# Optimization experiments

Measured on AMD Instinct MI355X. Metric: run time of the kernel, lower is better.

The kernel has to match this reference:

```python
import jax, jax.numpy as jnp
import numpy as np
import math

B, T, D = 2, 2048, 1024
H, HS = 16, 64  # n_heads, head_size; D == H*HS


def setup_inputs() -> dict:
    key = jax.random.key(0)
    k1, k2, k3 = jax.random.split(key, 3)
    x = jax.random.normal(k1, (B, T, D), dtype=jnp.float32)
    w_qkv = jax.random.normal(k2, (D, 3 * D), dtype=jnp.float32) * (1.0 / math.sqrt(D))
    b_qkv = jnp.zeros((3 * D,), dtype=jnp.float32)
    w_out = jax.random.normal(k3, (D, D), dtype=jnp.float32) * (1.0 / math.sqrt(D))
    b_out = jnp.zeros((D,), dtype=jnp.float32)
    return {"x": x, "w_qkv": w_qkv, "b_qkv": b_qkv, "w_out": w_out, "b_out": b_out}


def reference(x, w_qkv, b_qkv, w_out, b_out):
    b, t, d = x.shape
    qkv = x @ w_qkv + b_qkv                       # (B,T,3D)
    q, k, v = jnp.split(qkv, 3, axis=-1)
    # (B,T,D) -> (B,H,T,HS)
    q = q.reshape(b, t, H, HS).transpose(0, 2, 1, 3)
    k = k.reshape(b, t, H, HS).transpose(0, 2, 1, 3)
    v = v.reshape(b, t, H, HS).transpose(0, 2, 1, 3)
    scale = 1.0 / math.sqrt(HS)
    attn = jnp.einsum('bhqd,bhkd->bhqk', q, k) * scale  # (B,H,T,T)
    causal = jnp.tril(jnp.ones((t, t), dtype=bool))
    attn = jnp.where(causal[None, None], attn, -jnp.inf)
    attn = jax.nn.softmax(attn, axis=-1)
    o = jnp.einsum('bhqk,bhkd->bhqd', attn, v)          # (B,H,T,HS)
    o = o.transpose(0, 2, 1, 3).reshape(b, t, d)
    return o @ w_out + b_out
```

## Files before the change

kernel.cpp:

```cpp
#include <hip/hip_runtime.h>
#include <math.h>

#define B_  2
#define T_  2048
#define D_  1024
#define H_  16
#define HS_ 64
#define M_  (B_*T_)

typedef __bf16 bf16x8 __attribute__((ext_vector_type(8)));
typedef float  f32x4  __attribute__((ext_vector_type(4)));
typedef unsigned short u16;

static __device__ __forceinline__ u16 f2bf(float f) {
    __bf16 h = (__bf16)f;
    return *reinterpret_cast<u16*>(&h);
}

static __device__ __forceinline__ void glds16(const u16* g, u16* l) {
    __builtin_amdgcn_global_load_lds(
        (const __attribute__((address_space(1))) void*)g,
        (__attribute__((address_space(3))) void*)l, 16, 0, 0);
}

__global__ __launch_bounds__(256) void prep_kernel(
    const float* __restrict__ x, const float* __restrict__ w_qkv,
    const float* __restrict__ w_out,
    u16* __restrict__ Xb, u16* __restrict__ WqkvT, u16* __restrict__ WoutT)
{
    int bid = blockIdx.x;
    if (bid < 4096) {
        int i = (bid * 256 + threadIdx.x) * 4;
        float4 v = *reinterpret_cast<const float4*>(x + i);
        ushort4 o;
        o.x = f2bf(v.x); o.y = f2bf(v.y); o.z = f2bf(v.z); o.w = f2bf(v.w);
        *reinterpret_cast<ushort4*>(Xb + i) = o;
        return;
    }
    const float* in; u16* out; int C; int c0, r0;
    if (bid < 4096 + 3072) {
        int t = bid - 4096;
        in = w_qkv; out = WqkvT; C = 3 * D_;
        c0 = (t % 96) * 32; r0 = (t / 96) * 32;
    } else {
        int t = bid - 7168;
        in = w_out; out = WoutT; C = D_;
        c0 = (t & 31) * 32; r0 = (t >> 5) * 32;
    }
    __shared__ float tile[32][33];
    int tr = threadIdx.x >> 3, tc4 = (threadIdx.x & 7) * 4;
    float4 v = *reinterpret_cast<const float4*>(in + (size_t)(r0 + tr) * C + c0 + tc4);
    tile[tr][tc4+0] = v.x; tile[tr][tc4+1] = v.y;
    tile[tr][tc4+2] = v.z; tile[tr][tc4+3] = v.w;
    __syncthreads();
    ushort4 o;
    o.x = f2bf(tile[tc4+0][tr]); o.y = f2bf(tile[tc4+1][tr]);
    o.z = f2bf(tile[tc4+2][tr]); o.w = f2bf(tile[tc4+3][tr]);
    *reinterpret_cast<ushort4*>(out + (size_t)(c0 + tr) * D_ + r0 + tc4) = o;
}

__global__ __launch_bounds__(512, 2) void gemm_qkv(
    const u16* __restrict__ A, const u16* __restrict__ Bt,
    const float* __restrict__ bias,
    u16* __restrict__ Qb, u16* __restrict__ Kb, u16* __restrict__ Vt)
{
    constexpr int K  = D_;
    constexpr int NT = K / 64;

    __shared__ u16 LDS[2][2][2][8192];

    const int tid  = threadIdx.x;
    const int lane = tid & 63, wave = tid >> 6;
    const int wm = wave >> 2, wn = wave & 3;
    const int quad = lane >> 4, lr = lane & 15;

    const int lin = blockIdx.x + 16 * blockIdx.y;
    const int xcd = lin & 7, rr = lin >> 3;
    const int bm = (xcd & 3) * 4 + (rr & 3);
    const int bn = (xcd >> 2) * 6 + (rr >> 2);

    const u16* Ab = A  + (size_t)(bm * 256) * K;
    const u16* Bb = Bt + (size_t)(bn * 256) * K;

    const int r0 = tid >> 2;
    const int c0 = (tid & 3) ^ ((tid >> 3) & 3);
    const u16* sA0 = Ab + (size_t)r0 * K + c0 * 8;
    const u16* sA1 = sA0 + (size_t)128 * K;
    const u16* sB0 = Bb + (size_t)r0 * K + c0 * 8;
    const u16* sB1 = sB0 + (size_t)128 * K;
    const int d0 = tid * 8, d1 = (tid + 512) * 8;

    const int swz = (lr >> 1) & 3;
    const int eA = ((wm*128 + lr) * 4 + (quad ^ swz)) * 8;
    const int eB = ((wn*64  + lr) * 4 + (quad ^ swz)) * 8;

    f32x4 acc[8][4] = {};

#define STG(mat, kh, tt) do { \
        u16* _d = &LDS[(tt) & 1][mat][kh][0]; \
        const int _ko = (tt) * 64 + (kh) * 32; \
        glds16(((mat) ? sB0 : sA0) + _ko, _d + d0); \
        glds16(((mat) ? sB1 : sA1) + _ko, _d + d1); \
    } while (0)

#define MFMA_QUAD(mh) do { \
        __builtin_amdgcn_s_setprio(1); \
        _Pragma("unroll") \
        for (int i_ = 0; i_ < 4; ++i_) \
            _Pragma("unroll") \
            for (int j_ = 0; j_ < 4; ++j_) \
                acc[(mh)*4 + i_][j_] = __builtin_amdgcn_mfma_f32_16x16x32_bf16( \
                    a[i_], b[j_], acc[(mh)*4 + i_][j_], 0, 0, 0); \
        __builtin_amdgcn_s_setprio(0); \
    } while (0)

    STG(0,0,0); STG(1,0,0); STG(0,1,0); STG(1,1,0);
    asm volatile("s_waitcnt vmcnt(4)" ::: "memory");
    __builtin_amdgcn_s_barrier();

    for (int t = 0; t < NT; ++t) {
        const int cb = t & 1;
        const bool last = (t == NT - 1);
        const u16* Ar0 = &LDS[cb][0][0][0];
        const u16* Ar1 = &LDS[cb][0][1][0];
        const u16* Br0 = &LDS[cb][1][0][0];
        const u16* Br1 = &LDS[cb][1][1][0];
        bf16x8 a[4], b[4];

        #pragma unroll
        for (int i = 0; i < 4; ++i) a[i] = *reinterpret_cast<const bf16x8*>(Ar0 + eA + i*512);
        #pragma unroll
        for (int j = 0; j < 4; ++j) b[j] = *reinterpret_cast<const bf16x8*>(Br0 + eB + j*512);
        if (!last) STG(0,0,t+1);
        __builtin_amdgcn_s_barrier();
        asm volatile("s_waitcnt lgkmcnt(0)" ::: "memory");
        MFMA_QUAD(0);
        __builtin_amdgcn_s_barrier();

        #pragma unroll
        for (int i = 0; i < 4; ++i) a[i] = *reinterpret_cast<const bf16x8*>(Ar0 + eA + (i+4)*512);
        if (!last) STG(1,0,t+1);
        __builtin_amdgcn_s_barrier();
        asm volatile("s_waitcnt lgkmcnt(0)" ::: "memory");
        MFMA_QUAD(1);
        if (!last) { asm volatile("s_waitcnt vmcnt(4)" ::: "memory"); }
        else       { asm volatile("s_waitcnt vmcnt(0)" ::: "memory"); }
        __builtin_amdgcn_s_barrier();

        #pragma unroll
        for (int i = 0; i < 4; ++i) a[i] = *reinterpret_cast<const bf16x8*>(Ar1 + eA + i*512);
        #pragma unroll
        for (int j = 0; j < 4; ++j) b[j] = *reinterpret_cast<const bf16x8*>(Br1 + eB + j*512);
        if (!last) STG(0,1,t+1);
        __builtin_amdgcn_s_barrier();
        asm volatile("s_waitcnt lgkmcnt(0)" ::: "memory");
        MFMA_QUAD(0);
        __builtin_amdgcn_s_barrier();

        #pragma unroll
        for (int i = 0; i < 4; ++i) a[i] = *reinterpret_cast<const bf16x8*>(Ar1 + eA + (i+4)*512);
        if (!last) STG(1,1,t+1);
        __builtin_amdgcn_s_barrier();
        asm volatile("s_waitcnt lgkmcnt(0)" ::: "memory");
        MFMA_QUAD(1);
        asm volatile("s_waitcnt vmcnt(4)" ::: "memory");
        __builtin_amdgcn_s_barrier();
    }
#undef STG
#undef MFMA_QUAD

    #pragma unroll
    for (int i = 0; i < 8; ++i) {
        int m0 = bm*256 + wm*128 + i*16 + quad*4;
        #pragma unroll
        for (int j = 0; j < 4; ++j) {
            int ncol = bn*256 + wn*64 + j*16 + lr;
            float bv = bias[ncol];
            float v4[4];
            #pragma unroll
            for (int r = 0; r < 4; ++r) v4[r] = acc[i][j][r] + bv;
            int bb = m0 >> 11, t0 = m0 & (T_ - 1);
            int s = ncol >> 10, rem = ncol & 1023;
            int h = rem >> 6, d = rem & 63;
            int bh = bb * H_ + h;
            if (s == 0) {
                #pragma unroll
                for (int r = 0; r < 4; ++r)
                    Qb[((size_t)bh*T_ + t0 + r)*HS_ + d] = f2bf(v4[r] * 0.1803368801111244f);
            } else if (s == 1) {
                #pragma unroll
                for (int r = 0; r < 4; ++r)
                    Kb[((size_t)bh*T_ + t0 + r)*HS_ + d] = f2bf(v4[r]);
            } else {
                ushort4 o;
                o.x = f2bf(v4[0]); o.y = f2bf(v4[1]);
                o.z = f2bf(v4[2]); o.w = f2bf(v4[3]);
                *reinterpret_cast<ushort4*>(&Vt[((size_t)bh*HS_ + d)*T_ + t0]) = o;
            }
        }
    }
}

__global__ __launch_bounds__(256, 2) void gemm_out(
    const u16* __restrict__ A, const u16* __restrict__ Bt,
    const float* __restrict__ bias, float* __restrict__ Cf)
{
    constexpr int K  = D_;
    constexpr int N  = D_;
    constexpr int NT = K / 64;

    __shared__ u16 LDS[2][2][2][4096];

    const int tid  = threadIdx.x;
    const int lane = tid & 63, wave = tid >> 6;
    const int wm = wave >> 1, wn = wave & 1;
    const int quad = lane >> 4, lr = lane & 15;
    const int bm = blockIdx.x, bn = blockIdx.y;

    const u16* Ab = A  + (size_t)(bm * 128) * K;
    const u16* Bb = Bt + (size_t)(bn * 128) * K;

    const int r0 = tid >> 2;
    const int c0 = (tid & 3) ^ ((tid >> 3) & 3);
    const u16* sA0 = Ab + (size_t)r0 * K + c0 * 8;
    const u16* sA1 = sA0 + (size_t)64 * K;
    const u16* sB0 = Bb + (size_t)r0 * K + c0 * 8;
    const u16* sB1 = sB0 + (size_t)64 * K;
    const int d0 = tid * 8, d1 = (tid + 256) * 8;

    const int swz = (lr >> 1) & 3;
    const int eA = ((wm*64 + lr) * 4 + (quad ^ swz)) * 8;
    const int eB = ((wn*64 + lr) * 4 + (quad ^ swz)) * 8;

    f32x4 acc[4][4] = {};

#define STGO(kh, tt) do { \
        const int _ko = (tt) * 64 + (kh) * 32; \
        glds16(sA0 + _ko, &LDS[(tt) & 1][0][kh][0] + d0); \
        glds16(sA1 + _ko, &LDS[(tt) & 1][0][kh][0] + d1); \
        glds16(sB0 + _ko, &LDS[(tt) & 1][1][kh][0] + d0); \
        glds16(sB1 + _ko, &LDS[(tt) & 1][1][kh][0] + d1); \
    } while (0)

    STGO(0, 0); STGO(1, 0);
    asm volatile("s_waitcnt vmcnt(4)" ::: "memory");
    __builtin_amdgcn_s_barrier();

    for (int t = 0; t < NT; ++t) {
        const int cb = t & 1;
        const bool last = (t == NT - 1);
        bf16x8 a[4], b[4];

        {
            const u16* Ar = &LDS[cb][0][0][0];
            const u16* Br = &LDS[cb][1][0][0];
            #pragma unroll
            for (int i = 0; i < 4; ++i) a[i] = *reinterpret_cast<const bf16x8*>(Ar + eA + i*512);
            #pragma unroll
            for (int j = 0; j < 4; ++j) b[j] = *reinterpret_cast<const bf16x8*>(Br + eB + j*512);
            if (!last) STGO(0, t+1);
            __builtin_amdgcn_s_barrier();
            asm volatile("s_waitcnt lgkmcnt(0)" ::: "memory");
            __builtin_amdgcn_s_setprio(1);
            #pragma unroll
            for (int i = 0; i < 4; ++i)
                #pragma unroll
                for (int j = 0; j < 4; ++j)
                    acc[i][j] = __builtin_amdgcn_mfma_f32_16x16x32_bf16(a[i], b[j], acc[i][j], 0, 0, 0);
            __builtin_amdgcn_s_setprio(0);
            if (!last) { asm volatile("s_waitcnt vmcnt(4)" ::: "memory"); }
            else       { asm volatile("s_waitcnt vmcnt(0)" ::: "memory"); }
            __builtin_amdgcn_s_barrier();
        }

        {
            const u16* Ar = &LDS[cb][0][1][0];
            const u16* Br = &LDS[cb][1][1][0];
            #pragma unroll
            for (int i = 0; i < 4; ++i) a[i] = *reinterpret_cast<const bf16x8*>(Ar + eA + i*512);
            #pragma unroll
            for (int j = 0; j < 4; ++j) b[j] = *reinterpret_cast<const bf16x8*>(Br + eB + j*512);
            if (!last) STGO(1, t+1);
            __builtin_amdgcn_s_barrier();
            asm volatile("s_waitcnt lgkmcnt(0)" ::: "memory");
            __builtin_amdgcn_s_setprio(1);
            #pragma unroll
            for (int i = 0; i < 4; ++i)
                #pragma unroll
                for (int j = 0; j < 4; ++j)
                    acc[i][j] = __builtin_amdgcn_mfma_f32_16x16x32_bf16(a[i], b[j], acc[i][j], 0, 0, 0);
            __builtin_amdgcn_s_setprio(0);
            if (!last) { asm volatile("s_waitcnt vmcnt(4)" ::: "memory"); }
            __builtin_amdgcn_s_barrier();
        }
    }
#undef STGO

    #pragma unroll
    for (int i = 0; i < 4; ++i) {
        int m0 = bm*128 + wm*64 + i*16 + quad*4;
        #pragma unroll
        for (int j = 0; j < 4; ++j) {
            int ncol = bn*128 + wn*64 + j*16 + lr;
            float bv = bias[ncol];
            #pragma unroll
            for (int r = 0; r < 4; ++r)
                Cf[(size_t)(m0 + r) * N + ncol] = acc[i][j][r] + bv;
        }
    }
}

__global__ __launch_bounds__(256) void attn_kernel(
    const u16* __restrict__ Qb, const u16* __restrict__ Kb,
    const u16* __restrict__ Vt, u16* __restrict__ Ob)
{
    __shared__ u16 Ks[64 * 64];
    __shared__ u16 Vs[64 * 64];
    __shared__ u16 Ps[4][2][16 * 64];

    int tid  = threadIdx.x;
    int lane = tid & 63, wave = tid >> 6;
    int quad = lane >> 4, lr = lane & 15;

    int lin = blockIdx.x;
    int bh  = (lin & 7) + 8 * ((lin >> 3) & 3);
    int p   = lin >> 5;
    int qlo = p, qhi = 31 - p;
    int rlo = qlo * 64 + wave * 16;
    int rhi = qhi * 64 + wave * 16;

    const u16* QpL = Qb + ((size_t)bh * T_ + rlo) * HS_;
    const u16* QpH = Qb + ((size_t)bh * T_ + rhi) * HS_;
    bf16x8 qfL[2], qfH[2];
    #pragma unroll
    for (int h2 = 0; h2 < 2; ++h2) {
        qfL[h2] = *reinterpret_cast<const bf16x8*>(QpL + lr*HS_ + h2*32 + quad*8);
        qfH[h2] = *reinterpret_cast<const bf16x8*>(QpH + lr*HS_ + h2*32 + quad*8);
    }

    f32x4 OaL[4] = {}, OaH[4] = {};
    float lrL[4] = {0.f,0.f,0.f,0.f}, lrH[4] = {0.f,0.f,0.f,0.f};

    int e   = quad ^ (lr & 7);
    int rb0 = (lr * 8 + e) * 8;
    int rb1 = (lr * 8 + (e ^ 4)) * 8;
    int offw[4][4];
    #pragma unroll
    for (int nt = 0; nt < 4; ++nt)
        #pragma unroll
        for (int r = 0; r < 4; ++r) {
            int prow = quad*4 + r;
            offw[nt][r] = (prow*8 + ((nt*2 + (lr >> 3)) ^ (prow & 7)))*8 + (lr & 7);
        }
    u16* PsL = Ps[wave][0];
    u16* PsH = Ps[wave][1];

    int srow = tid >> 3;
    int scol = ((tid & 7) ^ (srow & 7)) * 8;
    const u16* kp0 = Kb + ((size_t)bh*T_ + srow     )*HS_ + scol;
    const u16* kp1 = Kb + ((size_t)bh*T_ + srow + 32)*HS_ + scol;
    const u16* vp0 = Vt + ((size_t)bh*HS_ + srow     )*T_ + scol;
    const u16* vp1 = Vt + ((size_t)bh*HS_ + srow + 32)*T_ + scol;

    bf16x8 kpre0 = *reinterpret_cast<const bf16x8*>(kp0);
    bf16x8 kpre1 = *reinterpret_cast<const bf16x8*>(kp1);
    bf16x8 vpre0 = *reinterpret_cast<const bf16x8*>(vp0);
    bf16x8 vpre1 = *reinterpret_cast<const bf16x8*>(vp1);

    for (int jt = 0; jt <= qhi; ++jt) {
        __syncthreads();
        reinterpret_cast<bf16x8*>(Ks)[tid]       = kpre0;
        reinterpret_cast<bf16x8*>(Ks)[tid + 256] = kpre1;
        reinterpret_cast<bf16x8*>(Vs)[tid]       = vpre0;
        reinterpret_cast<bf16x8*>(Vs)[tid + 256] = vpre1;
        if (jt < qhi) {
            kp0 += 64*HS_; kp1 += 64*HS_; vp0 += 64; vp1 += 64;
            kpre0 = *reinterpret_cast<const bf16x8*>(kp0);
            kpre1 = *reinterpret_cast<const bf16x8*>(kp1);
            vpre0 = *reinterpret_cast<const bf16x8*>(vp0);
            vpre1 = *reinterpret_cast<const bf16x8*>(vp1);
        }
        __syncthreads();

        const bool lo = (jt <= qlo);

        f32x4 SaH[4] = {}, SaL[4] = {};
        __builtin_amdgcn_s_setprio(1);
        #pragma unroll
        for (int nt = 0; nt < 4; ++nt) {
            bf16x8 bk0 = *reinterpret_cast<const bf16x8*>(Ks + rb0 + nt*1024);
            bf16x8 bk1 = *reinterpret_cast<const bf16x8*>(Ks + rb1 + nt*1024);
            SaH[nt] = __builtin_amdgcn_mfma_f32_16x16x32_bf16(qfH[0], bk0, SaH[nt], 0, 0, 0);
            SaH[nt] = __builtin_amdgcn_mfma_f32_16x16x32_bf16(qfH[1], bk1, SaH[nt], 0, 0, 0);
        }
        if (lo) {
            #pragma unroll
            for (int nt = 0; nt < 4; ++nt) {
                bf16x8 bk0 = *reinterpret_cast<const bf16x8*>(Ks + rb0 + nt*1024);
                bf16x8 bk1 = *reinterpret_cast<const bf16x8*>(Ks + rb1 + nt*1024);
                SaL[nt] = __builtin_amdgcn_mfma_f32_16x16x32_bf16(qfL[0], bk0, SaL[nt], 0, 0, 0);
                SaL[nt] = __builtin_amdgcn_mfma_f32_16x16x32_bf16(qfL[1], bk1, SaL[nt], 0, 0, 0);
            }
        }
        __builtin_amdgcn_s_setprio(0);

        if (jt == qhi) {
            int kb = jt * 64;
            #pragma unroll
            for (int nt = 0; nt < 4; ++nt)
                #pragma unroll
                for (int r = 0; r < 4; ++r) {
                    int kg = kb + nt*16 + lr;
                    int qg = rhi + quad*4 + r;
                    if (kg > qg) SaH[nt][r] = -INFINITY;
                }
        }
        if (jt == qlo) {
            int kb = jt * 64;
            #pragma unroll
            for (int nt = 0; nt < 4; ++nt)
                #pragma unroll
                for (int r = 0; r < 4; ++r) {
                    int kg = kb + nt*16 + lr;
                    int qg = rlo + quad*4 + r;
                    if (kg > qg) SaL[nt][r] = -INFINITY;
                }
        }

        #pragma unroll
        for (int nt = 0; nt < 4; ++nt)
            #pragma unroll
            for (int r = 0; r < 4; ++r) {
                float pv = __builtin_amdgcn_exp2f(SaH[nt][r]);
                lrH[r] += pv;
                PsH[offw[nt][r]] = f2bf(pv);
            }
        if (lo) {
            #pragma unroll
            for (int nt = 0; nt < 4; ++nt)
                #pragma unroll
                for (int r = 0; r < 4; ++r) {
                    float pv = __builtin_amdgcn_exp2f(SaL[nt][r]);
                    lrL[r] += pv;
                    PsL[offw[nt][r]] = f2bf(pv);
                }
        }

        __builtin_amdgcn_s_setprio(1);
        #pragma unroll
        for (int kk = 0; kk < 2; ++kk) {
            int rb = kk ? rb1 : rb0;
            bf16x8 pa = *reinterpret_cast<const bf16x8*>(PsH + rb);
            #pragma unroll
            for (int nt = 0; nt < 4; ++nt) {
                bf16x8 vb = *reinterpret_cast<const bf16x8*>(Vs + rb + nt*1024);
                OaH[nt] = __builtin_amdgcn_mfma_f32_16x16x32_bf16(pa, vb, OaH[nt], 0, 0, 0);
            }
        }
        if (lo) {
            #pragma unroll
            for (int kk = 0; kk < 2; ++kk) {
                int rb = kk ? rb1 : rb0;
                bf16x8 pa = *reinterpret_cast<const bf16x8*>(PsL + rb);
                #pragma unroll
                for (int nt = 0; nt < 4; ++nt) {
                    bf16x8 vb = *reinterpret_cast<const bf16x8*>(Vs + rb + nt*1024);
                    OaL[nt] = __builtin_amdgcn_mfma_f32_16x16x32_bf16(pa, vb, OaL[nt], 0, 0, 0);
                }
            }
        }
        __builtin_amdgcn_s_setprio(0);
    }

    int b = bh >> 4, h = bh & 15;
    #pragma unroll
    for (int r = 0; r < 4; ++r) {
        float sH = lrH[r], sL = lrL[r];
        #pragma unroll
        for (int off = 8; off >= 1; off >>= 1) {
            sH += __shfl_xor(sH, off, 64);
            sL += __shfl_xor(sL, off, 64);
        }
        float invH = 1.f / sH, invL = 1.f / sL;
        int qgH = rhi + quad*4 + r;
        int qgL = rlo + quad*4 + r;
        #pragma unroll
        for (int nt = 0; nt < 4; ++nt) {
            int d = nt*16 + lr;
            Ob[((size_t)b*T_ + qgH)*D_ + h*HS_ + d] = f2bf(OaH[nt][r] * invH);
            Ob[((size_t)b*T_ + qgL)*D_ + h*HS_ + d] = f2bf(OaL[nt][r] * invL);
        }
    }
}

extern "C" void kernel_launch(void* const* d_in, const int* in_sizes, int n_in,
                              void* d_out, int out_size, void* d_ws, size_t ws_size,
                              hipStream_t stream) {
    (void)in_sizes; (void)n_in; (void)out_size; (void)ws_size;
    const float* x     = (const float*)d_in[0];
    const float* w_qkv = (const float*)d_in[1];
    const float* b_qkv = (const float*)d_in[2];
    const float* w_out = (const float*)d_in[3];
    const float* b_out = (const float*)d_in[4];
    float* out = (float*)d_out;

    char* ws = (char*)d_ws;
    u16* Xb    = (u16*)ws; ws += (size_t)M_ * D_ * 2;
    u16* WqkvT = (u16*)ws; ws += (size_t)3 * D_ * D_ * 2;
    u16* WoutT = (u16*)ws; ws += (size_t)D_ * D_ * 2;
    u16* Qb    = (u16*)ws; ws += (size_t)M_ * D_ * 2;
    u16* Kb    = (u16*)ws; ws += (size_t)M_ * D_ * 2;
    u16* Vt    = (u16*)ws; ws += (size_t)M_ * D_ * 2;
    u16* Ob    = (u16*)ws; ws += (size_t)M_ * D_ * 2;

    prep_kernel<<<8192, 256, 0, stream>>>(x, w_qkv, w_out, Xb, WqkvT, WoutT);
    gemm_qkv<<<dim3(16, 12), 512, 0, stream>>>(
        Xb, WqkvT, b_qkv, Qb, Kb, Vt);
    attn_kernel<<<512, 256, 0, stream>>>(Qb, Kb, Vt, Ob);
    gemm_out<<<dim3(M_/128, D_/128), 256, 0, stream>>>(Ob, WoutT, b_out, out);
}
```

Before: 175.9 us.

## Double-buffer K/V tiles in LDS using direct global-to-LDS loads

Replaces the register-staged K/V prefetch with double-buffered LDS tiles filled by global_load_lds, issued one tile ahead. Each iteration now ends with one vmcnt wait and one barrier instead of two syncthreads around the LDS stores. This is meant to remove the VGPR round trip and a barrier per tile, at the cost of twice the K/V LDS footprint. The async loads write directly into the swizzled LDS layout, and the loop relies on the end-of-iteration wait and barrier to keep the two buffers from racing.

```diff
diff --git a/kernel.cpp b/kernel.cpp
--- a/kernel.cpp
+++ b/kernel.cpp
@@ -314,8 +314,8 @@
     const u16* __restrict__ Qb, const u16* __restrict__ Kb,
     const u16* __restrict__ Vt, u16* __restrict__ Ob)
 {
-    __shared__ u16 Ks[64 * 64];
-    __shared__ u16 Vs[64 * 64];
+    __shared__ u16 Ks[2][64 * 64];
+    __shared__ u16 Vs[2][64 * 64];
     __shared__ u16 Ps[4][2][16 * 64];
 
     int tid  = threadIdx.x;
@@ -362,42 +362,38 @@
     const u16* vp0 = Vt + ((size_t)bh*HS_ + srow     )*T_ + scol;
     const u16* vp1 = Vt + ((size_t)bh*HS_ + srow + 32)*T_ + scol;
 
-    bf16x8 kpre0 = *reinterpret_cast<const bf16x8*>(kp0);
-    bf16x8 kpre1 = *reinterpret_cast<const bf16x8*>(kp1);
-    bf16x8 vpre0 = *reinterpret_cast<const bf16x8*>(vp0);
-    bf16x8 vpre1 = *reinterpret_cast<const bf16x8*>(vp1);
+#define ASTG(buf) do { \
+        glds16(kp0, Ks[buf] + tid*8); glds16(kp1, Ks[buf] + (tid+256)*8); \
+        glds16(vp0, Vs[buf] + tid*8); glds16(vp1, Vs[buf] + (tid+256)*8); \
+        kp0 += 64*HS_; kp1 += 64*HS_; vp0 += 64; vp1 += 64; \
+    } while (0)
+
+    ASTG(0);
+    asm volatile("s_waitcnt vmcnt(0)" ::: "memory");
+    __builtin_amdgcn_s_barrier();
 
     for (int jt = 0; jt <= qhi; ++jt) {
-        __syncthreads();
-        reinterpret_cast<bf16x8*>(Ks)[tid]       = kpre0;
-        reinterpret_cast<bf16x8*>(Ks)[tid + 256] = kpre1;
-        reinterpret_cast<bf16x8*>(Vs)[tid]       = vpre0;
-        reinterpret_cast<bf16x8*>(Vs)[tid + 256] = vpre1;
-        if (jt < qhi) {
-            kp0 += 64*HS_; kp1 += 64*HS_; vp0 += 64; vp1 += 64;
-            kpre0 = *reinterpret_cast<const bf16x8*>(kp0);
-            kpre1 = *reinterpret_cast<const bf16x8*>(kp1);
-            vpre0 = *reinterpret_cast<const bf16x8*>(vp0);
-            vpre1 = *reinterpret_cast<const bf16x8*>(vp1);
-        }
-        __syncthreads();
-
+        const int cur = jt & 1;
+        if (jt < qhi) ASTG(cur ^ 1);
+
+        const u16* Kc = Ks[cur];
+        const u16* Vc = Vs[cur];
         const bool lo = (jt <= qlo);
 
         f32x4 SaH[4] = {}, SaL[4] = {};
         __builtin_amdgcn_s_setprio(1);
         #pragma unroll
         for (int nt = 0; nt < 4; ++nt) {
-            bf16x8 bk0 = *reinterpret_cast<const bf16x8*>(Ks + rb0 + nt*1024);
-            bf16x8 bk1 = *reinterpret_cast<const bf16x8*>(Ks + rb1 + nt*1024);
+            bf16x8 bk0 = *reinterpret_cast<const bf16x8*>(Kc + rb0 + nt*1024);
+            bf16x8 bk1 = *reinterpret_cast<const bf16x8*>(Kc + rb1 + nt*1024);
             SaH[nt] = __builtin_amdgcn_mfma_f32_16x16x32_bf16(qfH[0], bk0, SaH[nt], 0, 0, 0);
             SaH[nt] = __builtin_amdgcn_mfma_f32_16x16x32_bf16(qfH[1], bk1, SaH[nt], 0, 0, 0);
         }
         if (lo) {
             #pragma unroll
             for (int nt = 0; nt < 4; ++nt) {
-                bf16x8 bk0 = *reinterpret_cast<const bf16x8*>(Ks + rb0 + nt*1024);
-                bf16x8 bk1 = *reinterpret_cast<const bf16x8*>(Ks + rb1 + nt*1024);
+                bf16x8 bk0 = *reinterpret_cast<const bf16x8*>(Kc + rb0 + nt*1024);
+                bf16x8 bk1 = *reinterpret_cast<const bf16x8*>(Kc + rb1 + nt*1024);
                 SaL[nt] = __builtin_amdgcn_mfma_f32_16x16x32_bf16(qfL[0], bk0, SaL[nt], 0, 0, 0);
                 SaL[nt] = __builtin_amdgcn_mfma_f32_16x16x32_bf16(qfL[1], bk1, SaL[nt], 0, 0, 0);
             }
@@ -453,7 +449,7 @@
             bf16x8 pa = *reinterpret_cast<const bf16x8*>(PsH + rb);
             #pragma unroll
             for (int nt = 0; nt < 4; ++nt) {
-                bf16x8 vb = *reinterpret_cast<const bf16x8*>(Vs + rb + nt*1024);
+                bf16x8 vb = *reinterpret_cast<const bf16x8*>(Vc + rb + nt*1024);
                 OaH[nt] = __builtin_amdgcn_mfma_f32_16x16x32_bf16(pa, vb, OaH[nt], 0, 0, 0);
             }
         }
@@ -464,13 +460,17 @@
                 bf16x8 pa = *reinterpret_cast<const bf16x8*>(PsL + rb);
                 #pragma unroll
                 for (int nt = 0; nt < 4; ++nt) {
-                    bf16x8 vb = *reinterpret_cast<const bf16x8*>(Vs + rb + nt*1024);
+                    bf16x8 vb = *reinterpret_cast<const bf16x8*>(Vc + rb + nt*1024);
                     OaL[nt] = __builtin_amdgcn_mfma_f32_16x16x32_bf16(pa, vb, OaL[nt], 0, 0, 0);
                 }
             }
         }
         __builtin_amdgcn_s_setprio(0);
-    }
+
+        asm volatile("s_waitcnt vmcnt(0)" ::: "memory");
+        __builtin_amdgcn_s_barrier();
+    }
+#undef ASTG
 
     int b = bh >> 4, h = bh & 15;
     #pragma unroll
```

Measured after the change: 178.1 us. About the same (+1.2%).

## Split attention KV range across two blocks and merge partials

Applied to the files above, without the earlier changes.

Each query-tile pair is now handled by two blocks, each covering about half of the causal KV range. This doubles the attention grid to 1024 blocks to improve load balance and occupancy across CUs. Each block writes unnormalized fp32 partial outputs and row sums, and a new merge kernel adds the two halves, normalizes, and writes the bf16 output. The cost is extra fp32 global traffic, an extra kernel launch, and repeated Q loads.

```diff
diff --git a/kernel.cpp b/kernel.cpp
--- a/kernel.cpp
+++ b/kernel.cpp
@@ -312,7 +312,7 @@
 
 __global__ __launch_bounds__(256) void attn_kernel(
     const u16* __restrict__ Qb, const u16* __restrict__ Kb,
-    const u16* __restrict__ Vt, u16* __restrict__ Ob)
+    const u16* __restrict__ Vt, float* __restrict__ Op, float* __restrict__ Lp)
 {
     __shared__ u16 Ks[64 * 64];
     __shared__ u16 Vs[64 * 64];
@@ -324,8 +324,13 @@
 
     int lin = blockIdx.x;
     int bh  = (lin & 7) + 8 * ((lin >> 3) & 3);
-    int p   = lin >> 5;
+    int rest = lin >> 5;
+    int p   = rest & 15;
+    int hB  = rest >> 4;
     int qlo = p, qhi = 31 - p;
+    int s   = (p <= 7) ? (15 - p) : 8;
+    int j0  = hB ? s : 0;
+    int j1  = hB ? (qhi + 1) : s;
     int rlo = qlo * 64 + wave * 16;
     int rhi = qhi * 64 + wave * 16;
 
@@ -357,23 +362,23 @@
 
     int srow = tid >> 3;
     int scol = ((tid & 7) ^ (srow & 7)) * 8;
-    const u16* kp0 = Kb + ((size_t)bh*T_ + srow     )*HS_ + scol;
-    const u16* kp1 = Kb + ((size_t)bh*T_ + srow + 32)*HS_ + scol;
-    const u16* vp0 = Vt + ((size_t)bh*HS_ + srow     )*T_ + scol;
-    const u16* vp1 = Vt + ((size_t)bh*HS_ + srow + 32)*T_ + scol;
+    const u16* kp0 = Kb + ((size_t)bh*T_ + j0*64 + srow     )*HS_ + scol;
+    const u16* kp1 = Kb + ((size_t)bh*T_ + j0*64 + srow + 32)*HS_ + scol;
+    const u16* vp0 = Vt + ((size_t)bh*HS_ + srow     )*T_ + j0*64 + scol;
+    const u16* vp1 = Vt + ((size_t)bh*HS_ + srow + 32)*T_ + j0*64 + scol;
 
     bf16x8 kpre0 = *reinterpret_cast<const bf16x8*>(kp0);
     bf16x8 kpre1 = *reinterpret_cast<const bf16x8*>(kp1);
     bf16x8 vpre0 = *reinterpret_cast<const bf16x8*>(vp0);
     bf16x8 vpre1 = *reinterpret_cast<const bf16x8*>(vp1);
 
-    for (int jt = 0; jt <= qhi; ++jt) {
+    for (int jt = j0; jt < j1; ++jt) {
         __syncthreads();
         reinterpret_cast<bf16x8*>(Ks)[tid]       = kpre0;
         reinterpret_cast<bf16x8*>(Ks)[tid + 256] = kpre1;
         reinterpret_cast<bf16x8*>(Vs)[tid]       = vpre0;
         reinterpret_cast<bf16x8*>(Vs)[tid + 256] = vpre1;
-        if (jt < qhi) {
+        if (jt + 1 < j1) {
             kp0 += 64*HS_; kp1 += 64*HS_; vp0 += 64; vp1 += 64;
             kpre0 = *reinterpret_cast<const bf16x8*>(kp0);
             kpre1 = *reinterpret_cast<const bf16x8*>(kp1);
@@ -472,7 +477,8 @@
         __builtin_amdgcn_s_setprio(0);
     }
 
-    int b = bh >> 4, h = bh & 15;
+    float* OpB = Op + ((size_t)hB * 32 + bh) * T_ * HS_;
+    float* LpB = Lp + ((size_t)hB * 32 + bh) * T_;
     #pragma unroll
     for (int r = 0; r < 4; ++r) {
         float sH = lrH[r], sL = lrL[r];
@@ -481,16 +487,40 @@
             sH += __shfl_xor(sH, off, 64);
             sL += __shfl_xor(sL, off, 64);
         }
-        float invH = 1.f / sH, invL = 1.f / sL;
         int qgH = rhi + quad*4 + r;
         int qgL = rlo + quad*4 + r;
+        if (lr == 0) {
+            LpB[qgH] = sH;
+            LpB[qgL] = sL;
+        }
         #pragma unroll
         for (int nt = 0; nt < 4; ++nt) {
             int d = nt*16 + lr;
-            Ob[((size_t)b*T_ + qgH)*D_ + h*HS_ + d] = f2bf(OaH[nt][r] * invH);
-            Ob[((size_t)b*T_ + qgL)*D_ + h*HS_ + d] = f2bf(OaL[nt][r] * invL);
-        }
-    }
+            OpB[(size_t)qgH*HS_ + d] = OaH[nt][r];
+            OpB[(size_t)qgL*HS_ + d] = OaL[nt][r];
+        }
+    }
+}
+
+__global__ __launch_bounds__(256) void merge_kernel(
+    const float* __restrict__ Op, const float* __restrict__ Lp,
+    u16* __restrict__ Ob)
+{
+    int idx = blockIdx.x * 256 + threadIdx.x;
+    int e0  = idx * 4;
+    int row = e0 >> 6;
+    int d0  = e0 & 63;
+    float4 v0 = *reinterpret_cast<const float4*>(Op + (size_t)e0);
+    float4 v1 = *reinterpret_cast<const float4*>(Op + (size_t)e0 + (size_t)32*T_*HS_);
+    float inv = 1.f / (Lp[row] + Lp[row + 32*T_]);
+    int bh = row >> 11, q = row & 2047;
+    int b = bh >> 4, hh = bh & 15;
+    ushort4 o;
+    o.x = f2bf((v0.x + v1.x) * inv);
+    o.y = f2bf((v0.y + v1.y) * inv);
+    o.z = f2bf((v0.z + v1.z) * inv);
+    o.w = f2bf((v0.w + v1.w) * inv);
+    *reinterpret_cast<ushort4*>(Ob + ((size_t)(b*T_ + q))*D_ + hh*HS_ + d0) = o;
 }
 
 extern "C" void kernel_launch(void* const* d_in, const int* in_sizes, int n_in,
@@ -512,10 +542,13 @@
     u16* Kb    = (u16*)ws; ws += (size_t)M_ * D_ * 2;
     u16* Vt    = (u16*)ws; ws += (size_t)M_ * D_ * 2;
     u16* Ob    = (u16*)ws; ws += (size_t)M_ * D_ * 2;
+    float* Op  = (float*)ws; ws += (size_t)2 * M_ * D_ * 4;
+    float* Lp  = (float*)ws; ws += (size_t)2 * M_ * 16 * 4;
 
     prep_kernel<<<8192, 256, 0, stream>>>(x, w_qkv, w_out, Xb, WqkvT, WoutT);
     gemm_qkv<<<dim3(16, 12), 512, 0, stream>>>(
         Xb, WqkvT, b_qkv, Qb, Kb, Vt);
-    attn_kernel<<<512, 256, 0, stream>>>(Qb, Kb, Vt, Ob);
+    attn_kernel<<<1024, 256, 0, stream>>>(Qb, Kb, Vt, Op, Lp);
+    merge_kernel<<<4096, 256, 0, stream>>>(Op, Lp, Ob);
     gemm_out<<<dim3(M_/128, D_/128), 256, 0, stream>>>(Ob, WoutT, b_out, out);
 }
```

Result: slower. 184.1 us (+4.6%).

## Transpose QK^T MFMA operands so P rows land in lanes for packed writes

Applied to the files above, without the earlier changes.

Swaps the A/B operands of the QK^T MFMA so each lane holds four consecutive keys of a single query row. Probabilities can then be packed pairwise into bf16 with v_cvt_pk_bf16_f32 and written to LDS as 8-byte stores instead of scalar 2-byte stores. Row sums become one scalar per lane, reduced with two shuffles at the end and redistributed by lane shuffle. The high and low MFMA loops are also interleaved to share K and V fragment loads. The result depends on the new swizzled offsets matching the PV read layout, and inline asm limits compiler scheduling.

```diff
diff --git a/kernel.cpp b/kernel.cpp
--- a/kernel.cpp
+++ b/kernel.cpp
@@ -11,6 +11,7 @@
 typedef __bf16 bf16x8 __attribute__((ext_vector_type(8)));
 typedef float  f32x4  __attribute__((ext_vector_type(4)));
 typedef unsigned short u16;
+typedef unsigned int u32;
 
 static __device__ __forceinline__ u16 f2bf(float f) {
     __bf16 h = (__bf16)f;
@@ -339,19 +340,15 @@
     }
 
     f32x4 OaL[4] = {}, OaH[4] = {};
-    float lrL[4] = {0.f,0.f,0.f,0.f}, lrH[4] = {0.f,0.f,0.f,0.f};
+    float lsumL = 0.f, lsumH = 0.f;
 
     int e   = quad ^ (lr & 7);
     int rb0 = (lr * 8 + e) * 8;
     int rb1 = (lr * 8 + (e ^ 4)) * 8;
-    int offw[4][4];
+    int off64[4];
     #pragma unroll
     for (int nt = 0; nt < 4; ++nt)
-        #pragma unroll
-        for (int r = 0; r < 4; ++r) {
-            int prow = quad*4 + r;
-            offw[nt][r] = (prow*8 + ((nt*2 + (lr >> 3)) ^ (prow & 7)))*8 + (lr & 7);
-        }
+        off64[nt] = (lr*8 + ((2*nt + (quad >> 1)) ^ (lr & 7)))*8 + (quad & 1)*4;
     u16* PsL = Ps[wave][0];
     u16* PsH = Ps[wave][1];
 
@@ -390,98 +387,93 @@
         for (int nt = 0; nt < 4; ++nt) {
             bf16x8 bk0 = *reinterpret_cast<const bf16x8*>(Ks + rb0 + nt*1024);
             bf16x8 bk1 = *reinterpret_cast<const bf16x8*>(Ks + rb1 + nt*1024);
-            SaH[nt] = __builtin_amdgcn_mfma_f32_16x16x32_bf16(qfH[0], bk0, SaH[nt], 0, 0, 0);
-            SaH[nt] = __builtin_amdgcn_mfma_f32_16x16x32_bf16(qfH[1], bk1, SaH[nt], 0, 0, 0);
-        }
-        if (lo) {
-            #pragma unroll
-            for (int nt = 0; nt < 4; ++nt) {
-                bf16x8 bk0 = *reinterpret_cast<const bf16x8*>(Ks + rb0 + nt*1024);
-                bf16x8 bk1 = *reinterpret_cast<const bf16x8*>(Ks + rb1 + nt*1024);
-                SaL[nt] = __builtin_amdgcn_mfma_f32_16x16x32_bf16(qfL[0], bk0, SaL[nt], 0, 0, 0);
-                SaL[nt] = __builtin_amdgcn_mfma_f32_16x16x32_bf16(qfL[1], bk1, SaL[nt], 0, 0, 0);
+            SaH[nt] = __builtin_amdgcn_mfma_f32_16x16x32_bf16(bk0, qfH[0], SaH[nt], 0, 0, 0);
+            SaH[nt] = __builtin_amdgcn_mfma_f32_16x16x32_bf16(bk1, qfH[1], SaH[nt], 0, 0, 0);
+            if (lo) {
+                SaL[nt] = __builtin_amdgcn_mfma_f32_16x16x32_bf16(bk0, qfL[0], SaL[nt], 0, 0, 0);
+                SaL[nt] = __builtin_amdgcn_mfma_f32_16x16x32_bf16(bk1, qfL[1], SaL[nt], 0, 0, 0);
             }
         }
         __builtin_amdgcn_s_setprio(0);
 
         if (jt == qhi) {
-            int kb = jt * 64;
             #pragma unroll
             for (int nt = 0; nt < 4; ++nt)
                 #pragma unroll
                 for (int r = 0; r < 4; ++r) {
-                    int kg = kb + nt*16 + lr;
-                    int qg = rhi + quad*4 + r;
+                    int kg = jt*64 + nt*16 + quad*4 + r;
+                    int qg = rhi + lr;
                     if (kg > qg) SaH[nt][r] = -INFINITY;
                 }
         }
         if (jt == qlo) {
-            int kb = jt * 64;
             #pragma unroll
             for (int nt = 0; nt < 4; ++nt)
                 #pragma unroll
                 for (int r = 0; r < 4; ++r) {
-                    int kg = kb + nt*16 + lr;
-                    int qg = rlo + quad*4 + r;
+                    int kg = jt*64 + nt*16 + quad*4 + r;
+                    int qg = rlo + lr;
                     if (kg > qg) SaL[nt][r] = -INFINITY;
                 }
         }
 
         #pragma unroll
-        for (int nt = 0; nt < 4; ++nt)
-            #pragma unroll
-            for (int r = 0; r < 4; ++r) {
-                float pv = __builtin_amdgcn_exp2f(SaH[nt][r]);
-                lrH[r] += pv;
-                PsH[offw[nt][r]] = f2bf(pv);
+        for (int nt = 0; nt < 4; ++nt) {
+            float e0 = __builtin_amdgcn_exp2f(SaH[nt][0]);
+            float e1 = __builtin_amdgcn_exp2f(SaH[nt][1]);
+            float e2 = __builtin_amdgcn_exp2f(SaH[nt][2]);
+            float e3 = __builtin_amdgcn_exp2f(SaH[nt][3]);
+            lsumH += (e0 + e1) + (e2 + e3);
+            u32 d0, d1;
+            asm("v_cvt_pk_bf16_f32 %0, %1, %2" : "=v"(d0) : "v"(e0), "v"(e1));
+            asm("v_cvt_pk_bf16_f32 %0, %1, %2" : "=v"(d1) : "v"(e2), "v"(e3));
+            uint2 w; w.x = d0; w.y = d1;
+            *reinterpret_cast<uint2*>(PsH + off64[nt]) = w;
+        }
+        if (lo) {
+            #pragma unroll
+            for (int nt = 0; nt < 4; ++nt) {
+                float e0 = __builtin_amdgcn_exp2f(SaL[nt][0]);
+                float e1 = __builtin_amdgcn_exp2f(SaL[nt][1]);
+                float e2 = __builtin_amdgcn_exp2f(SaL[nt][2]);
+                float e3 = __builtin_amdgcn_exp2f(SaL[nt][3]);
+                lsumL += (e0 + e1) + (e2 + e3);
+                u32 d0, d1;
+                asm("v_cvt_pk_bf16_f32 %0, %1, %2" : "=v"(d0) : "v"(e0), "v"(e1));
+                asm("v_cvt_pk_bf16_f32 %0, %1, %2" : "=v"(d1) : "v"(e2), "v"(e3));
+                uint2 w; w.x = d0; w.y = d1;
+                *reinterpret_cast<uint2*>(PsL + off64[nt]) = w;
             }
-        if (lo) {
-            #pragma unroll
-            for (int nt = 0; nt < 4; ++nt)
-                #pragma unroll
-                for (int r = 0; r < 4; ++r) {
-                    float pv = __builtin_amdgcn_exp2f(SaL[nt][r]);
-                    lrL[r] += pv;
-                    PsL[offw[nt][r]] = f2bf(pv);
-                }
         }
 
         __builtin_amdgcn_s_setprio(1);
         #pragma unroll
         for (int kk = 0; kk < 2; ++kk) {
             int rb = kk ? rb1 : rb0;
-            bf16x8 pa = *reinterpret_cast<const bf16x8*>(PsH + rb);
+            bf16x8 paH = *reinterpret_cast<const bf16x8*>(PsH + rb);
+            bf16x8 paL = *reinterpret_cast<const bf16x8*>(PsL + rb);
             #pragma unroll
             for (int nt = 0; nt < 4; ++nt) {
                 bf16x8 vb = *reinterpret_cast<const bf16x8*>(Vs + rb + nt*1024);
-                OaH[nt] = __builtin_amdgcn_mfma_f32_16x16x32_bf16(pa, vb, OaH[nt], 0, 0, 0);
+                OaH[nt] = __builtin_amdgcn_mfma_f32_16x16x32_bf16(paH, vb, OaH[nt], 0, 0, 0);
+                if (lo)
+                    OaL[nt] = __builtin_amdgcn_mfma_f32_16x16x32_bf16(paL, vb, OaL[nt], 0, 0, 0);
             }
         }
-        if (lo) {
-            #pragma unroll
-            for (int kk = 0; kk < 2; ++kk) {
-                int rb = kk ? rb1 : rb0;
-                bf16x8 pa = *reinterpret_cast<const bf16x8*>(PsL + rb);
-                #pragma unroll
-                for (int nt = 0; nt < 4; ++nt) {
-                    bf16x8 vb = *reinterpret_cast<const bf16x8*>(Vs + rb + nt*1024);
-                    OaL[nt] = __builtin_amdgcn_mfma_f32_16x16x32_bf16(pa, vb, OaL[nt], 0, 0, 0);
-                }
-            }
-        }
         __builtin_amdgcn_s_setprio(0);
     }
 
     int b = bh >> 4, h = bh & 15;
+    float sH = lsumH;
+    sH += __shfl_xor(sH, 16, 64);
+    sH += __shfl_xor(sH, 32, 64);
+    float sL = lsumL;
+    sL += __shfl_xor(sL, 16, 64);
+    sL += __shfl_xor(sL, 32, 64);
     #pragma unroll
     for (int r = 0; r < 4; ++r) {
-        float sH = lrH[r], sL = lrL[r];
-        #pragma unroll
-        for (int off = 8; off >= 1; off >>= 1) {
-            sH += __shfl_xor(sH, off, 64);
-            sL += __shfl_xor(sL, off, 64);
-        }
-        float invH = 1.f / sH, invL = 1.f / sL;
+        float invH = 1.f / __shfl(sH, quad*4 + r, 64);
+        float invL = 1.f / __shfl(sL, quad*4 + r, 64);
         int qgH = rhi + quad*4 + r;
         int qgL = rlo + quad*4 + r;
         #pragma unroll
```

New measurement: 177.0 us. No clear change (+0.6%).
